# Kernel tuning notes

Measured on AMD Instinct MI355X. Metric: run time of the kernel, lower is better.

## Reference

```python
import jax, jax.numpy as jnp
import numpy as np

B, T1, T2 = 8, 512, 128
LA = 128            # len_alphabet
E = LA // 2         # embedding_size = GRU units = conv channels
DL = 256            # lstm_outs feature dim


def gru_seq(x, mask, K, R, b):
    """Keras GRU (reset_after=True) with masking. x:(B,T,E) mask:(B,T) -> (B,T,U)."""
    u = R.shape[0]
    xg = jnp.einsum('bte,eu->btu', x, K) + b[0]  # precompute input gates (B,T,3U)

    def step(carry, inp):
        h, y_prev = carry
        xt, mt = inp
        rg = h @ R + b[1]
        xz, xr, xh = jnp.split(xt, 3, axis=-1)
        rz, rr, rh = jnp.split(rg, 3, axis=-1)
        z = jax.nn.sigmoid(xz + rz)
        r = jax.nn.sigmoid(xr + rr)
        hh = jnp.tanh(xh + r * rh)
        h_new = z * h + (1.0 - z) * hh
        m = mt[:, None]
        h_out = jnp.where(m, h_new, h)
        y = jnp.where(m, h_new, y_prev)  # masked steps copy previous output
        return (h_out, y), y

    h0 = jnp.zeros((x.shape[0], u), x.dtype)
    _, ys = jax.lax.scan(step, (h0, h0), (jnp.swapaxes(xg, 0, 1), mask.T))
    return jnp.swapaxes(ys, 0, 1)


def setup_inputs() -> dict:
    key = jax.random.key(0)
    ks = jax.random.split(key, 15)
    s = 0.05
    inp = {
        'lstm_outs': jax.random.normal(ks[0], (B, T1, DL), jnp.float32),
        'char_seq': jax.random.randint(ks[1], (B, T2), 1, LA + 1, jnp.int32),  # no pad -> mask all True
        'emb_table': jax.random.normal(ks[2], (LA + 1, E), jnp.float32) * s,
        'Kf': jax.random.normal(ks[3], (E, 3 * E), jnp.float32) * s,
        'Rf': jax.random.normal(ks[4], (E, 3 * E), jnp.float32) * s,
        'bf': jnp.zeros((2, 3 * E), jnp.float32),
        'Kb': jax.random.normal(ks[5], (E, 3 * E), jnp.float32) * s,
        'Rb': jax.random.normal(ks[6], (E, 3 * E), jnp.float32) * s,
        'bb': jnp.zeros((2, 3 * E), jnp.float32),
        'w_char': jax.random.normal(ks[7], (DL + 2 * E + 2, 1), jnp.float32) * s,
        'b_char': jnp.zeros((1,), jnp.float32),
        'conv1_w': jax.random.normal(ks[8], (2, 2 * E, E), jnp.float32) * s,
        'conv1_b': jnp.zeros((E,), jnp.float32),
        'conv2_w': jax.random.normal(ks[9], (2, E, E), jnp.float32) * s,
        'conv2_b': jnp.zeros((E,), jnp.float32),
    }
    return inp


def reference(lstm_outs, char_seq, emb_table, Kf, Rf, bf, Kb, Rb, bb,
              w_char, b_char, conv1_w, conv1_b, conv2_w, conv2_b):
    emb = emb_table[char_seq]                 # (B,T2,E)
    mask = char_seq != 0
    fwd = gru_seq(emb, mask, Kf, Rf, bf)
    bwd = gru_seq(emb[:, ::-1], mask[:, ::-1], Kb, Rb, bb)[:, ::-1]
    ctx = jnp.concatenate([fwd, bwd], axis=-1)  # (B,T2,2E) contexted_chars

    t1, t2 = lstm_outs.shape[1], ctx.shape[1]
    dl, dc = lstm_outs.shape[2], ctx.shape[2]
    # Dense(1) over concat([lstms, contexts, time_idx, char_idx]) decomposed per part
    w_l = w_char[:dl, 0]
    w_c = w_char[dl:dl + dc, 0]
    w_t = w_char[dl + dc, 0]
    w_i = w_char[dl + dc + 1, 0]
    score = (jnp.einsum('btd,d->bt', lstm_outs, w_l)[:, :, None]
             + jnp.einsum('bsd,d->bs', ctx, w_c)[:, None, :]
             + w_t * jnp.arange(t1, dtype=lstm_outs.dtype)[None, :, None]
             + w_i * jnp.arange(t2, dtype=lstm_outs.dtype)[None, None, :]
             + b_char[0])
    char_weights = score[..., None]           # (B,T1,T2,1)

    weighted = char_weights * ctx[:, None, :, :]  # (B,T1,T2,2E)
    # Conv1D kernel=2, valid, over char axis (-2)
    c1 = (jnp.einsum('btsc,co->btso', weighted[:, :, :-1], conv1_w[0])
          + jnp.einsum('btsc,co->btso', weighted[:, :, 1:], conv1_w[1]) + conv1_b)
    c2 = (jnp.einsum('btsc,co->btso', c1[:, :, :-1], conv2_w[0])
          + jnp.einsum('btsc,co->btso', c1[:, :, 1:], conv2_w[1]) + conv2_b)
    final_embedding = jnp.max(c2, axis=-2)    # (B,T1,E)
    return final_embedding, char_weights
```

## Files before the change

kernel.cpp:

```cpp
#include <hip/hip_runtime.h>
#include <hip/hip_bf16.h>
#include <math.h>

#define Bn 8
#define T1n 512
#define T2n 128
#define En 64
#define Gn 192
#define DLn 256

#define NEG_LOG2E  (-1.4426950408889634f)
#define TWO_LOG2E  (2.8853900817779268f)

typedef __attribute__((ext_vector_type(8))) short short8;
typedef __attribute__((ext_vector_type(4))) float float4v;

__device__ __forceinline__ float fast_rcp(float x) { return __builtin_amdgcn_rcpf(x); }

__device__ __forceinline__ float fast_exp2(float x) {
    float r;
    asm("v_exp_f32 %0, %1" : "=v"(r) : "v"(x));
    return r;
}

__device__ __forceinline__ unsigned short f32_to_bf16(float v) {
    unsigned u = __builtin_bit_cast(unsigned, v);
    u += 0x7FFFu + ((u >> 16) & 1u);
    return (unsigned short)(u >> 16);
}
__device__ __forceinline__ float bf16_to_f32(unsigned short s) {
    unsigned u = ((unsigned)s) << 16;
    return __builtin_bit_cast(float, u);
}

__device__ __forceinline__ void load_lds16(const void* g, void* l) {
    __builtin_amdgcn_global_load_lds(
        (const __attribute__((address_space(1))) unsigned int*)g,
        (__attribute__((address_space(3))) unsigned int*)l, 16, 0, 0);
}

__global__ __launch_bounds__(384) void k_pre(const int* __restrict__ char_seq,
                                             const float* __restrict__ emb_table,
                                             const float* __restrict__ Kf,
                                             const float* __restrict__ bf,
                                             const float* __restrict__ Kb,
                                             const float* __restrict__ bb,
                                             unsigned short* __restrict__ xgbf) {
    int bt = blockIdx.x;
    int b = bt >> 7, t = bt & 127;
    int tid = threadIdx.x;
    __shared__ __align__(16) float emb[En];
    if (tid < En) {
        int cs = char_seq[b * T2n + t];
        emb[tid] = emb_table[cs * En + tid];
    }
    __syncthreads();
    int d = tid / Gn;
    int j = tid - d * Gn;
    const float* K = d ? Kb : Kf;
    const float* bias = d ? bb : bf;
    float acc = bias[j];
    #pragma unroll
    for (int e = 0; e < En; ++e) acc = fmaf(emb[e], K[e * Gn + j], acc);
    if (j < 128) acc *= NEG_LOG2E;
    xgbf[((size_t)(d * Bn + b) * T2n + t) * Gn + j] = f32_to_bf16(acc);
}

__global__ __launch_bounds__(64) void k_scan(const unsigned short* __restrict__ xgbf,
                                             const float* __restrict__ Rf,
                                             const float* __restrict__ bf,
                                             const float* __restrict__ Rb,
                                             const float* __restrict__ bb,
                                             const int* __restrict__ char_seq,
                                             float* __restrict__ ctx) {
    int blk = blockIdx.x;
    int b = blk & 7, d = blk >> 3;
    int lane = threadIdx.x;
    int quad = lane >> 4, col = lane & 15;

    __shared__ __align__(16) unsigned short xg_l[T2n * Gn];
    __shared__ __align__(16) unsigned short hb[En];

    {
        const unsigned char* gb = (const unsigned char*)(xgbf + (size_t)(d * Bn + b) * T2n * Gn);
        unsigned char* lb = (unsigned char*)xg_l;
        #pragma unroll
        for (int i = 0; i < 48; ++i)
            load_lds16(gb + i * 1024 + lane * 16, lb + i * 1024 + lane * 16);
    }

    unsigned long long mlo = __ballot(char_seq[b * T2n + lane] != 0);
    unsigned long long mhi = __ballot(char_seq[b * T2n + 64 + lane] != 0);

    const float* R = d ? Rb : Rf;
    const float* bias = d ? bb : bf;
    short8 frag[12][2];
    #pragma unroll
    for (int nt = 0; nt < 12; ++nt)
        #pragma unroll
        for (int kt = 0; kt < 2; ++kt) {
            short8 f;
            #pragma unroll
            for (int j = 0; j < 8; ++j) {
                float v = R[(kt * 32 + quad * 8 + j) * Gn + nt * 16 + col];
                if (nt < 8) v *= NEG_LOG2E;
                f[j] = (short)f32_to_bf16(v);
            }
            frag[nt][kt] = f;
        }
    float bz = bias[Gn + lane] * NEG_LOG2E;
    float br = bias[Gn + En + lane] * NEG_LOG2E;
    float bh = bias[Gn + 2 * En + lane];

    hb[lane] = 0;
    float hreg = 0.f, y = 0.f;
    float* ctxb = ctx + (size_t)b * T2n * 128 + d * En;
    int i0 = d ? (T2n - 1) : 0;
    int istep = d ? -1 : 1;
    bool q1 = (quad & 1) != 0, q2 = (quad & 2) != 0;
    const short8* ap = (const short8*)hb;

    asm volatile("s_waitcnt vmcnt(0)" ::: "memory");

    for (int step = 0; step < T2n; ++step) {
        int idx = i0 + istep * step;
        short8 a0 = ap[quad];
        short8 a1 = ap[4 + quad];
        int xb = idx * Gn + lane;
        unsigned short xzs = xg_l[xb];
        unsigned short xrs = xg_l[xb + 64];
        unsigned short xhs = xg_l[xb + 128];
        float4v z4 = {0.f, 0.f, 0.f, 0.f};
        float4v acc[12];
        #pragma unroll
        for (int nt = 0; nt < 12; ++nt) {
            float4v p = __builtin_amdgcn_mfma_f32_16x16x32_bf16(a0, frag[nt][0], z4, 0, 0, 0);
            acc[nt] = __builtin_amdgcn_mfma_f32_16x16x32_bf16(a1, frag[nt][1], p, 0, 0, 0);
        }
        float rz = (q2 ? (q1 ? acc[3].x : acc[2].x) : (q1 ? acc[1].x : acc[0].x)) + bz;
        float rr = (q2 ? (q1 ? acc[7].x : acc[6].x) : (q1 ? acc[5].x : acc[4].x)) + br;
        float rh = (q2 ? (q1 ? acc[11].x : acc[10].x) : (q1 ? acc[9].x : acc[8].x)) + bh;
        float xz = bf16_to_f32(xzs), xr = bf16_to_f32(xrs), xh = bf16_to_f32(xhs);
        float z = fast_rcp(1.f + fast_exp2(xz + rz));
        float r = fast_rcp(1.f + fast_exp2(xr + rr));
        float a = fmaf(r, rh, xh);
        float hh = fmaf(-2.f, fast_rcp(1.f + fast_exp2(a * TWO_LOG2E)), 1.f);
        float hn = fmaf(z, hreg - hh, hh);
        bool m = (idx < 64) ? ((mlo >> idx) & 1ull) : ((mhi >> (idx - 64)) & 1ull);
        if (m) { hreg = hn; y = hn; }
        ctxb[idx * 128 + lane] = y;
        hb[lane] = f32_to_bf16(hreg);
    }
}

__global__ __launch_bounds__(128) void k_ctxw(const float* __restrict__ ctx,
                                              const float* __restrict__ conv1_w,
                                              const float* __restrict__ conv2_w,
                                              const float* __restrict__ w_char,
                                              const float* __restrict__ lstm,
                                              float* __restrict__ Am,
                                              float* __restrict__ Bm,
                                              float* __restrict__ Cm,
                                              float* __restrict__ sC,
                                              float* __restrict__ sL) {
    int bs = blockIdx.x;
    int tid = threadIdx.x;
    {
        int wv = tid >> 6, lane = tid & 63;
        const float4* wl = (const float4*)w_char;
        #pragma unroll
        for (int q = 0; q < 2; ++q) {
            int bt = bs * 4 + wv * 2 + q;
            const float4* row = (const float4*)(lstm + (size_t)bt * DLn);
            float4 r4 = row[lane];
            float4 w4 = wl[lane];
            float s = r4.x * w4.x + r4.y * w4.y + r4.z * w4.z + r4.w * w4.w;
            #pragma unroll
            for (int off = 32; off; off >>= 1) s += __shfl_down(s, off);
            if (lane == 0) sL[bt] = s;
        }
    }
    __shared__ float crow[128];
    __shared__ float p0[En], p1[En];
    crow[tid] = ctx[(size_t)bs * 128 + tid];
    __syncthreads();
    if (tid < 64) {
        float s = crow[tid] * w_char[DLn + tid] + crow[64 + tid] * w_char[DLn + 64 + tid];
        #pragma unroll
        for (int off = 32; off; off >>= 1) s += __shfl_down(s, off);
        if (tid == 0) sC[bs] = s;
    }
    int tap = tid >> 6, o = tid & 63;
    const float* W = conv1_w + tap * 128 * En;
    float acc = 0.f;
    #pragma unroll
    for (int c = 0; c < 128; ++c) acc = fmaf(crow[c], W[c * En + o], acc);
    if (tap == 0) p0[o] = acc; else p1[o] = acc;
    __syncthreads();
    const float* W20 = conv2_w;
    const float* W21 = conv2_w + En * En;
    if (tid < 64) {
        float a = 0.f, cm = 0.f;
        #pragma unroll
        for (int c = 0; c < En; ++c) {
            a  = fmaf(p0[c], W20[c * En + tid], a);
            cm = fmaf(p1[c], W21[c * En + tid], cm);
        }
        Am[(size_t)bs * En + tid] = a;
        Cm[(size_t)bs * En + tid] = cm;
    } else {
        int o2 = tid - 64;
        float bacc = 0.f;
        #pragma unroll
        for (int c = 0; c < En; ++c) {
            bacc = fmaf(p1[c], W20[c * En + o2], bacc);
            bacc = fmaf(p0[c], W21[c * En + o2], bacc);
        }
        Bm[(size_t)bs * En + o2] = bacc;
    }
}

__global__ __launch_bounds__(128) void k_final(const float* __restrict__ sL,
                                               const float* __restrict__ sC,
                                               const float* __restrict__ w_char,
                                               const float* __restrict__ b_char,
                                               const float* __restrict__ conv1_b,
                                               const float* __restrict__ conv2_w,
                                               const float* __restrict__ conv2_b,
                                               const float* __restrict__ Am,
                                               const float* __restrict__ Bm,
                                               const float* __restrict__ Cm,
                                               float* __restrict__ fe,
                                               float* __restrict__ cw) {
    int blk = blockIdx.x;
    int b = blk >> 6, ttile = blk & 63;
    int t0 = ttile * 8;
    int tid = threadIdx.x;
    float w_t = w_char[DLn + 128], w_i = w_char[DLn + 129], bc = b_char[0];
    __shared__ float sc8[8][T2n];
    {
        int s = tid;
        float sCs = sC[b * T2n + s] + w_i * (float)s + bc;
        #pragma unroll
        for (int tt = 0; tt < 8; ++tt) {
            int t = t0 + tt;
            float v = sL[b * T1n + t] + sCs + w_t * (float)t;
            sc8[tt][s] = v;
            cw[((size_t)(b * T1n + t)) * T2n + s] = v;
        }
    }
    int o = tid & 63, p = tid >> 6;
    float bb2 = conv2_b[o];
    #pragma unroll
    for (int c = 0; c < En; ++c)
        bb2 += conv1_b[c] * (conv2_w[c * En + o] + conv2_w[En * En + c * En + o]);
    __syncthreads();

    float acc[8];
    #pragma unroll
    for (int tt = 0; tt < 8; ++tt) acc[tt] = -__builtin_inff();
    const float* Ab = Am + (size_t)(b * T2n) * En + o;
    const float* Bb = Bm + (size_t)(b * T2n) * En + o;
    const float* Cb = Cm + (size_t)(b * T2n) * En + o;
    for (int s = p; s < T2n - 2; s += 2) {
        float a  = Ab[s * En];
        float bm = Bb[(s + 1) * En];
        float cm = Cb[(s + 2) * En];
        #pragma unroll
        for (int tt = 0; tt < 8; ++tt) {
            float v = fmaf(sc8[tt][s], a,
                      fmaf(sc8[tt][s + 1], bm,
                      fmaf(sc8[tt][s + 2], cm, bb2)));
            acc[tt] = fmaxf(acc[tt], v);
        }
    }
    __shared__ float red[64][9];
    if (p == 1) {
        #pragma unroll
        for (int tt = 0; tt < 8; ++tt) red[o][tt] = acc[tt];
    }
    __syncthreads();
    if (p == 0) {
        #pragma unroll
        for (int tt = 0; tt < 8; ++tt) {
            float v = fmaxf(acc[tt], red[o][tt]);
            fe[((size_t)(b * T1n + t0 + tt)) * En + o] = v;
        }
    }
}

extern "C" void kernel_launch(void* const* d_in, const int* in_sizes, int n_in,
                              void* d_out, int out_size, void* d_ws, size_t ws_size,
                              hipStream_t stream) {
    const float* lstm      = (const float*)d_in[0];
    const int*   char_seq  = (const int*)d_in[1];
    const float* emb_table = (const float*)d_in[2];
    const float* Kf        = (const float*)d_in[3];
    const float* Rf        = (const float*)d_in[4];
    const float* bf        = (const float*)d_in[5];
    const float* Kb        = (const float*)d_in[6];
    const float* Rb        = (const float*)d_in[7];
    const float* bb        = (const float*)d_in[8];
    const float* w_char    = (const float*)d_in[9];
    const float* b_char    = (const float*)d_in[10];
    const float* conv1_w   = (const float*)d_in[11];
    const float* conv1_b   = (const float*)d_in[12];
    const float* conv2_w   = (const float*)d_in[13];
    const float* conv2_b   = (const float*)d_in[14];

    float* out = (float*)d_out;
    float* fe = out;
    float* cw = out + Bn * T1n * En;

    float* ws  = (float*)d_ws;
    unsigned short* xgbf = (unsigned short*)ws;
    float* ctx = ws + 98304;
    float* sC  = ctx + Bn * T2n * 128;
    float* sL  = sC + Bn * T2n;
    float* Am  = sL + Bn * T1n;
    float* Bm  = Am + Bn * T2n * En;
    float* Cm  = Bm + Bn * T2n * En;

    k_pre <<<Bn * T2n, 384, 0, stream>>>(char_seq, emb_table, Kf, bf, Kb, bb, xgbf);
    k_scan<<<16, 64, 0, stream>>>(xgbf, Rf, bf, Rb, bb, char_seq, ctx);
    k_ctxw<<<Bn * T2n, 128, 0, stream>>>(ctx, conv1_w, conv2_w, w_char, lstm,
                                         Am, Bm, Cm, sC, sL);
    k_final<<<(Bn * T1n) / 8, 128, 0, stream>>>(sL, sC, w_char, b_char, conv1_b,
                                                conv2_w, conv2_b, Am, Bm, Cm, fe, cw);
}
```

Measured before the change: 169.1 us.

## Split GRU scan recurrence across four wavefronts with double-buffered hidden state

```diff
diff --git a/kernel.cpp b/kernel.cpp
--- a/kernel.cpp
+++ b/kernel.cpp
@@ -66,27 +66,33 @@
     xgbf[((size_t)(d * Bn + b) * T2n + t) * Gn + j] = f32_to_bf16(acc);
 }
 
-__global__ __launch_bounds__(64) void k_scan(const unsigned short* __restrict__ xgbf,
-                                             const float* __restrict__ Rf,
-                                             const float* __restrict__ bf,
-                                             const float* __restrict__ Rb,
-                                             const float* __restrict__ bb,
-                                             const int* __restrict__ char_seq,
-                                             float* __restrict__ ctx) {
+__global__ __launch_bounds__(256) void k_scan(const unsigned short* __restrict__ xgbf,
+                                              const float* __restrict__ Rf,
+                                              const float* __restrict__ bf,
+                                              const float* __restrict__ Rb,
+                                              const float* __restrict__ bb,
+                                              const int* __restrict__ char_seq,
+                                              float* __restrict__ ctx) {
     int blk = blockIdx.x;
     int b = blk & 7, d = blk >> 3;
-    int lane = threadIdx.x;
+    int tid = threadIdx.x;
+    int w = tid >> 6;
+    int lane = tid & 63;
     int quad = lane >> 4, col = lane & 15;
+    int u = w * 16 + col;
 
     __shared__ __align__(16) unsigned short xg_l[T2n * Gn];
-    __shared__ __align__(16) unsigned short hb[En];
+    __shared__ __align__(16) unsigned short h0[En];
+    __shared__ __align__(16) unsigned short h1[En];
 
     {
         const unsigned char* gb = (const unsigned char*)(xgbf + (size_t)(d * Bn + b) * T2n * Gn);
         unsigned char* lb = (unsigned char*)xg_l;
         #pragma unroll
-        for (int i = 0; i < 48; ++i)
-            load_lds16(gb + i * 1024 + lane * 16, lb + i * 1024 + lane * 16);
+        for (int i = 0; i < 12; ++i) {
+            int o = (w * 12 + i) * 1024 + lane * 16;
+            load_lds16(gb + o, lb + o);
+        }
     }
 
     unsigned long long mlo = __ballot(char_seq[b * T2n + lane] != 0);
@@ -94,63 +100,77 @@
 
     const float* R = d ? Rb : Rf;
     const float* bias = d ? bb : bf;
-    short8 frag[12][2];
-    #pragma unroll
-    for (int nt = 0; nt < 12; ++nt)
+    short8 frag[3][2];
+    float4v biasC[3];
+    #pragma unroll
+    for (int g = 0; g < 3; ++g) {
+        int nt = g * 4 + w;
         #pragma unroll
         for (int kt = 0; kt < 2; ++kt) {
             short8 f;
             #pragma unroll
             for (int j = 0; j < 8; ++j) {
                 float v = R[(kt * 32 + quad * 8 + j) * Gn + nt * 16 + col];
-                if (nt < 8) v *= NEG_LOG2E;
+                if (g < 2) v *= NEG_LOG2E;
                 f[j] = (short)f32_to_bf16(v);
             }
-            frag[nt][kt] = f;
-        }
-    float bz = bias[Gn + lane] * NEG_LOG2E;
-    float br = bias[Gn + En + lane] * NEG_LOG2E;
-    float bh = bias[Gn + 2 * En + lane];
-
-    hb[lane] = 0;
+            frag[g][kt] = f;
+        }
+        float bv = bias[Gn + nt * 16 + col];
+        if (g < 2) bv *= NEG_LOG2E;
+        float4v c = {bv, 0.f, 0.f, 0.f};
+        biasC[g] = c;
+    }
+
+    if (tid < En) h0[tid] = 0;
     float hreg = 0.f, y = 0.f;
     float* ctxb = ctx + (size_t)b * T2n * 128 + d * En;
     int i0 = d ? (T2n - 1) : 0;
     int istep = d ? -1 : 1;
-    bool q1 = (quad & 1) != 0, q2 = (quad & 2) != 0;
-    const short8* ap = (const short8*)hb;
-
-    asm volatile("s_waitcnt vmcnt(0)" ::: "memory");
-
-    for (int step = 0; step < T2n; ++step) {
-        int idx = i0 + istep * step;
-        short8 a0 = ap[quad];
-        short8 a1 = ap[4 + quad];
-        int xb = idx * Gn + lane;
-        unsigned short xzs = xg_l[xb];
-        unsigned short xrs = xg_l[xb + 64];
-        unsigned short xhs = xg_l[xb + 128];
-        float4v z4 = {0.f, 0.f, 0.f, 0.f};
-        float4v acc[12];
-        #pragma unroll
-        for (int nt = 0; nt < 12; ++nt) {
-            float4v p = __builtin_amdgcn_mfma_f32_16x16x32_bf16(a0, frag[nt][0], z4, 0, 0, 0);
-            acc[nt] = __builtin_amdgcn_mfma_f32_16x16x32_bf16(a1, frag[nt][1], p, 0, 0, 0);
-        }
-        float rz = (q2 ? (q1 ? acc[3].x : acc[2].x) : (q1 ? acc[1].x : acc[0].x)) + bz;
-        float rr = (q2 ? (q1 ? acc[7].x : acc[6].x) : (q1 ? acc[5].x : acc[4].x)) + br;
-        float rh = (q2 ? (q1 ? acc[11].x : acc[10].x) : (q1 ? acc[9].x : acc[8].x)) + bh;
-        float xz = bf16_to_f32(xzs), xr = bf16_to_f32(xrs), xh = bf16_to_f32(xhs);
-        float z = fast_rcp(1.f + fast_exp2(xz + rz));
-        float r = fast_rcp(1.f + fast_exp2(xr + rr));
-        float a = fmaf(r, rh, xh);
-        float hh = fmaf(-2.f, fast_rcp(1.f + fast_exp2(a * TWO_LOG2E)), 1.f);
-        float hn = fmaf(z, hreg - hh, hh);
-        bool m = (idx < 64) ? ((mlo >> idx) & 1ull) : ((mhi >> (idx - 64)) & 1ull);
-        if (m) { hreg = hn; y = hn; }
-        ctxb[idx * 128 + lane] = y;
-        hb[lane] = f32_to_bf16(hreg);
-    }
+
+    asm volatile("s_waitcnt vmcnt(0) lgkmcnt(0)" ::: "memory");
+    __builtin_amdgcn_s_barrier();
+    __builtin_amdgcn_sched_barrier(0);
+
+    #define SCAN_STEP(CUR, NXT, STEP)                                              \
+    {                                                                              \
+        int idx = i0 + istep * (STEP);                                             \
+        const short8* ap = (const short8*)(CUR);                                   \
+        short8 a0 = ap[quad];                                                      \
+        short8 a1 = ap[4 + quad];                                                  \
+        int xb = idx * Gn + u;                                                     \
+        unsigned short xzs = xg_l[xb];                                             \
+        unsigned short xrs = xg_l[xb + 64];                                        \
+        unsigned short xhs = xg_l[xb + 128];                                       \
+        float4v aZ = __builtin_amdgcn_mfma_f32_16x16x32_bf16(a0, frag[0][0], biasC[0], 0, 0, 0); \
+        float4v aR = __builtin_amdgcn_mfma_f32_16x16x32_bf16(a0, frag[1][0], biasC[1], 0, 0, 0); \
+        float4v aH = __builtin_amdgcn_mfma_f32_16x16x32_bf16(a0, frag[2][0], biasC[2], 0, 0, 0); \
+        aZ = __builtin_amdgcn_mfma_f32_16x16x32_bf16(a1, frag[0][1], aZ, 0, 0, 0); \
+        aR = __builtin_amdgcn_mfma_f32_16x16x32_bf16(a1, frag[1][1], aR, 0, 0, 0); \
+        aH = __builtin_amdgcn_mfma_f32_16x16x32_bf16(a1, frag[2][1], aH, 0, 0, 0); \
+        float xz = bf16_to_f32(xzs), xr = bf16_to_f32(xrs), xh = bf16_to_f32(xhs); \
+        float z = fast_rcp(1.f + fast_exp2(xz + aZ.x));                            \
+        float r = fast_rcp(1.f + fast_exp2(xr + aR.x));                            \
+        float a = fmaf(r, aH.x, xh);                                               \
+        float hh = fmaf(-2.f, fast_rcp(1.f + fast_exp2(a * TWO_LOG2E)), 1.f);      \
+        float hn = fmaf(z, hreg - hh, hh);                                         \
+        bool m = (idx < 64) ? ((mlo >> idx) & 1ull) : ((mhi >> (idx - 64)) & 1ull);\
+        if (m) { hreg = hn; y = hn; }                                              \
+        if (quad == 0) {                                                           \
+            ctxb[idx * 128 + u] = y;                                               \
+            (NXT)[u] = f32_to_bf16(hreg);                                          \
+        }                                                                          \
+        asm volatile("s_waitcnt lgkmcnt(0)" ::: "memory");                         \
+        __builtin_amdgcn_sched_barrier(0);                                         \
+        __builtin_amdgcn_s_barrier();                                              \
+        __builtin_amdgcn_sched_barrier(0);                                         \
+    }
+
+    for (int sp = 0; sp < T2n / 2; ++sp) {
+        SCAN_STEP(h0, h1, 2 * sp);
+        SCAN_STEP(h1, h0, 2 * sp + 1);
+    }
+    #undef SCAN_STEP
 }
 
 __global__ __launch_bounds__(128) void k_ctxw(const float* __restrict__ ctx,
@@ -322,7 +342,7 @@
     float* Cm  = Bm + Bn * T2n * En;
 
     k_pre <<<Bn * T2n, 384, 0, stream>>>(char_seq, emb_table, Kf, bf, Kb, bb, xgbf);
-    k_scan<<<16, 64, 0, stream>>>(xgbf, Rf, bf, Rb, bb, char_seq, ctx);
+    k_scan<<<16, 256, 0, stream>>>(xgbf, Rf, bf, Rb, bb, char_seq, ctx);
     k_ctxw<<<Bn * T2n, 128, 0, stream>>>(ctx, conv1_w, conv2_w, w_char, lstm,
                                          Am, Bm, Cm, sC, sL);
     k_final<<<(Bn * T1n) / 8, 128, 0, stream>>>(sL, sC, w_char, b_char, conv1_b,
```

Result: faster. 150.3 us (-11.1%).
